# Performance work log

Measured on AMD Instinct MI355X. Metric: run time of the kernel, lower is better.

## Reference

```python
import jax, jax.numpy as jnp
import numpy as np

B, N = 1, 512
NODE_DIM, EDGE_DIM = 384, 128
H, SK, SV, PK, PV = 8, 16, 16, 4, 4
EPS = 1e-8
LN_EPS = 1e-5


def setup_inputs() -> dict:
    key = jax.random.key(0)
    ks = jax.random.split(key, 20)
    d, e = NODE_DIM, EDGE_DIM
    s = 0.02
    rn = lambda k, sh: jax.random.normal(k, sh, jnp.float32) * s
    # orthonormal per-residue rotations (valid rigid frames)
    R, _ = jnp.linalg.qr(jax.random.normal(ks[2], (B, N, 3, 3), jnp.float32))
    out_dim = H * (SV + EDGE_DIM + PV * 4)  # scalar + pairwise + points(3) + point norms(1)
    return dict(
        node_features=jax.random.normal(ks[0], (B, N, d), jnp.float32),
        edge_features=jax.random.normal(ks[1], (B, N, N, e), jnp.float32),
        rotations=R,
        translations=jax.random.normal(ks[3], (B, N, 3), jnp.float32),
        mask=jnp.ones((B, N), bool),
        Wq_s=rn(ks[4], (d, H * SK)), Wk_s=rn(ks[5], (d, H * SK)), Wv_s=rn(ks[6], (d, H * SV)),
        Wq_p=rn(ks[7], (d, H * PK * 3)), Wk_p=rn(ks[8], (d, H * PK * 3)), Wv_p=rn(ks[9], (d, H * PV * 3)),
        point_weights=jnp.full((H,), np.log(np.e - 1.0), jnp.float32),  # softplus -> 1
        Wb=rn(ks[10], (e, H)), bb=jnp.zeros((H,), jnp.float32),
        Wo=rn(ks[11], (out_dim, d)), bo=jnp.zeros((d,), jnp.float32),
        g1=jnp.ones((d,), jnp.float32), beta1=jnp.zeros((d,), jnp.float32),
        W1=rn(ks[12], (d, 2 * d)), b1=jnp.zeros((2 * d,), jnp.float32),
        W2=rn(ks[13], (2 * d, 2 * d)), b2=jnp.zeros((2 * d,), jnp.float32),
        W3=rn(ks[14], (2 * d, d)), b3=jnp.zeros((d,), jnp.float32),
        g2=jnp.ones((d,), jnp.float32), beta2=jnp.zeros((d,), jnp.float32),
    )


def _layer_norm(x, g, b):
    mu = x.mean(-1, keepdims=True)
    var = ((x - mu) ** 2).mean(-1, keepdims=True)
    return (x - mu) * jax.lax.rsqrt(var + LN_EPS) * g + b


def _forward(node_features, edge_features, rotations, translations, mask,
             Wq_s, Wk_s, Wv_s, Wq_p, Wk_p, Wv_p, point_weights, Wb, bb, Wo, bo,
             g1, beta1, W1, b1, W2, b2, W3, b3, g2, beta2):
    b, n, d = node_features.shape
    # num_attn_logits = 3 (scalar + point + pairwise)
    scal_scale = (3 * SK) ** -0.5
    point_scale = (3 * PK * 4.5) ** -0.5
    pair_scale = 3 ** -0.5

    qs = (node_features @ Wq_s).reshape(b, n, H, SK)
    kk = (node_features @ Wk_s).reshape(b, n, H, SK)
    vs = (node_features @ Wv_s).reshape(b, n, H, SV)

    def apply_rigid(p):  # p: (b,n,h,d,3); global = R^T applied per lucidrains einsum + t
        return jnp.einsum('bnhdc,bncr->bnhdr', p, rotations) + translations[:, :, None, None, :]

    qp = apply_rigid((node_features @ Wq_p).reshape(b, n, H, PK, 3))
    kp = apply_rigid((node_features @ Wk_p).reshape(b, n, H, PK, 3))
    vp = apply_rigid((node_features @ Wv_p).reshape(b, n, H, PV, 3))

    logits = jnp.einsum('bihk,bjhk->bhij', qs, kk) * scal_scale

    # point distance term: sum_{d,c} (q-k)^2 = |q|^2 + |k|^2 - 2 q.k (avoids (b,h,i,j,d,3) tensor)
    w = jax.nn.softplus(point_weights)  # (H,)
    q2 = jnp.einsum('bnhdc,bnhdc->bhn', qp, qp)
    k2 = jnp.einsum('bnhdc,bnhdc->bhn', kp, kp)
    cross = jnp.einsum('bihdc,bjhdc->bhij', qp, kp)
    dist = q2[..., :, None] + k2[..., None, :] - 2.0 * cross  # (b,h,i,j)
    logits = logits - 0.5 * point_scale * w[None, :, None, None] * dist

    pair_bias = (jnp.einsum('bije,eh->bhij', edge_features, Wb) + bb[None, :, None, None]) * pair_scale
    logits = logits + pair_bias

    pm = mask[:, None, :, None] & mask[:, None, None, :]  # (b,1,i,j)
    logits = jnp.where(pm, logits, -jnp.finfo(logits.dtype).max)
    attn = jax.nn.softmax(logits, axis=-1)  # (b,h,i,j)

    rs = jnp.einsum('bhij,bjhv->bihv', attn, vs).reshape(b, n, H * SV)
    rp = jnp.einsum('bhij,bije->bihe', attn, edge_features).reshape(b, n, H * EDGE_DIM)
    pts = jnp.einsum('bhij,bjhdc->bihdc', attn, vp)
    # invert rigid: subtract t, apply R (inverse of R^T application)
    local = jnp.einsum('bihdc,birc->bihdr', pts - translations[:, :, None, None, :], rotations)
    norms = jnp.sqrt((local ** 2).sum(-1) + EPS)  # (b,n,H,PV)

    cat = jnp.concatenate([rs, local.reshape(b, n, H * PV * 3), norms.reshape(b, n, H * PV), rp], axis=-1)
    ipa_out = cat @ Wo + bo

    x = _layer_norm(ipa_out, g1, beta1)  # dropout is identity at eval
    x = jax.nn.relu(x @ W1 + b1)
    x = jax.nn.relu(x @ W2 + b2)
    x = x @ W3 + b3
    return _layer_norm(x, g2, beta2)


def reference(node_features, edge_features, rotations, translations, mask,
              Wq_s, Wk_s, Wv_s, Wq_p, Wk_p, Wv_p, point_weights, Wb, bb, Wo, bo,
              g1, beta1, W1, b1, W2, b2, W3, b3, g2, beta2):
    return _forward(node_features, edge_features, rotations, translations, mask,
                    Wq_s, Wk_s, Wv_s, Wq_p, Wk_p, Wv_p, point_weights, Wb, bb, Wo, bo,
                    g1, beta1, W1, b1, W2, b2, W3, b3, g2, beta2)
```

## Files before the change

### kernel.cpp

```cpp
#include <hip/hip_runtime.h>
#include <cstddef>

#define NN 512
#define DD 384
#define EE 128
#define HH 8

static constexpr float SCAL_SCALE  = 0.1443375673f;
static constexpr float POINT_SCALE = 0.1360827635f;
static constexpr float PAIR_SCALE  = 0.5773502692f;
static constexpr float LN_EPS = 1e-5f;
static constexpr float EPS    = 1e-8f;

typedef __bf16 bf16x8 __attribute__((ext_vector_type(8)));
typedef float  f32x4  __attribute__((ext_vector_type(4)));

__device__ __forceinline__ unsigned short bf16_bits(float v) {
    union { __bf16 b; unsigned short s; } c; c.b = (__bf16)v; return c.s;
}
__device__ __forceinline__ float bits2f(unsigned u) {
    union { unsigned u; float f; } c; c.u = u; return c.f;
}

__global__ __launch_bounds__(256) void prep_weights_kernel(
    const float* __restrict__ Wo, const float* __restrict__ W1,
    const float* __restrict__ W2, const float* __restrict__ W3,
    const float* __restrict__ Wq_s, const float* __restrict__ Wk_s,
    const float* __restrict__ Wv_s,
    const float* __restrict__ Wq_p, const float* __restrict__ Wk_p,
    const float* __restrict__ Wv_p,
    unsigned short* __restrict__ WoT, unsigned short* __restrict__ W1T,
    unsigned short* __restrict__ W2T, unsigned short* __restrict__ W3T,
    unsigned short* __restrict__ WprojT)
{
    const int b = blockIdx.x;
    const float* W; unsigned short* out;
    int K, N, tile, rowoff = 0;
    if (b < 480)       { W = Wo;   out = WoT;    K = 1280; N = 384; tile = b; }
    else if (b < 768)  { W = W1;   out = W1T;    K = 384;  N = 768; tile = b - 480; }
    else if (b < 1344) { W = W2;   out = W2T;    K = 768;  N = 768; tile = b - 768; }
    else if (b < 1632) { W = W3;   out = W3T;    K = 768;  N = 384; tile = b - 1344; }
    else if (b < 1680) { W = Wq_s; out = WprojT; K = 384;  N = 128; tile = b - 1632; rowoff = 0; }
    else if (b < 1728) { W = Wk_s; out = WprojT; K = 384;  N = 128; tile = b - 1680; rowoff = 128; }
    else if (b < 1776) { W = Wv_s; out = WprojT; K = 384;  N = 128; tile = b - 1728; rowoff = 256; }
    else if (b < 1812) { W = Wq_p; out = WprojT; K = 384;  N = 96;  tile = b - 1776; rowoff = 384; }
    else if (b < 1848) { W = Wk_p; out = WprojT; K = 384;  N = 96;  tile = b - 1812; rowoff = 480; }
    else               { W = Wv_p; out = WprojT; K = 384;  N = 96;  tile = b - 1848; rowoff = 576; }

    const int ntn = N / 32;
    const int n0 = (tile % ntn) * 32, k0 = (tile / ntn) * 32;
    __shared__ float tb[32][33];
    const int tx = threadIdx.x & 31, ty = threadIdx.x >> 5;
    #pragma unroll
    for (int dy = 0; dy < 32; dy += 8)
        tb[ty + dy][tx] = W[(size_t)(k0 + ty + dy) * N + n0 + tx];
    __syncthreads();
    #pragma unroll
    for (int dy = 0; dy < 32; dy += 8)
        out[(size_t)(rowoff + n0 + ty + dy) * K + k0 + tx] = bf16_bits(tb[tx][ty + dy]);
}

template <int K, int NOUT, bool RELU, bool HASB>
__global__ __launch_bounds__(256) void gemm_mfma2(
    const float* __restrict__ X, const unsigned short* __restrict__ Wt,
    const float* __restrict__ bias, float* __restrict__ Y)
{
    const int t = threadIdx.x;
    const int w = t >> 6, lane = t & 63;
    const int r = lane & 15, q = lane >> 4;
    const int n0 = blockIdx.x * 16;
    const int m0 = blockIdx.y * 64;

    __shared__ unsigned short Xs[64 * 40];
    __shared__ unsigned short Ws[16 * 40];

    const int row_s = t >> 2, seg_s = t & 3;
    f32x4 acc = {0.f, 0.f, 0.f, 0.f};

    for (int ks = 0; ks < K / 32; ks++) {
        __syncthreads();
        {
            const float* src = X + (size_t)(m0 + row_s) * K + ks * 32 + seg_s * 8;
            float4 a = *(const float4*)src;
            float4 b = *(const float4*)(src + 4);
            union { bf16x8 v; uint4 u; } pk;
            pk.v[0] = (__bf16)a.x; pk.v[1] = (__bf16)a.y;
            pk.v[2] = (__bf16)a.z; pk.v[3] = (__bf16)a.w;
            pk.v[4] = (__bf16)b.x; pk.v[5] = (__bf16)b.y;
            pk.v[6] = (__bf16)b.z; pk.v[7] = (__bf16)b.w;
            *(uint4*)&Xs[row_s * 40 + seg_s * 8] = pk.u;
            if (t < 64)
                *(uint4*)&Ws[row_s * 40 + seg_s * 8] =
                    *(const uint4*)&Wt[(size_t)(n0 + row_s) * K + ks * 32 + seg_s * 8];
        }
        __syncthreads();
        bf16x8 a = *(const bf16x8*)&Xs[(w * 16 + r) * 40 + q * 8];
        bf16x8 b = *(const bf16x8*)&Ws[r * 40 + q * 8];
        acc = __builtin_amdgcn_mfma_f32_16x16x32_bf16(a, b, acc, 0, 0, 0);
    }
    const float bi = HASB ? bias[n0 + r] : 0.f;
    #pragma unroll
    for (int reg = 0; reg < 4; reg++) {
        const int m = m0 + w * 16 + q * 4 + reg;
        float v = acc[reg] + bi;
        if (RELU) v = fmaxf(v, 0.f);
        Y[(size_t)m * NOUT + n0 + r] = v;
    }
}

__global__ __launch_bounds__(256) void ipa_post_kernel(
    const float* __restrict__ proj_out, const float* __restrict__ rot,
    const float* __restrict__ trans, const float* __restrict__ pw,
    const float* __restrict__ bb,
    unsigned short* __restrict__ Qp, unsigned short* __restrict__ Kp,
    unsigned short* __restrict__ svT)
{
    const int i = blockIdx.x;
    const int t = threadIdx.x;
    __shared__ float outs[672];
    __shared__ float ptg[288];
    __shared__ float q2s[8], k2s[8], pwh[8];

    for (int f = t; f < 672; f += 256) outs[f] = proj_out[(size_t)i * 672 + f];
    if (t < 8) pwh[t] = 0.5f * POINT_SCALE * log1pf(expf(pw[t]));
    __syncthreads();

    for (int f = t; f < 288; f += 256) {
        int which = f / 96, idx = f % 96;
        int hd = idx / 3, r = idx % 3;
        float acc = trans[(size_t)i * 3 + r];
        #pragma unroll
        for (int c = 0; c < 3; c++)
            acc += outs[384 + which * 96 + hd * 3 + c] * rot[(size_t)i * 9 + c * 3 + r];
        ptg[f] = acc;
    }
    __syncthreads();
    if (t < 16) {
        int which = t / 8, h = t % 8;
        float acc = 0.f;
        #pragma unroll
        for (int m = 0; m < 12; m++) {
            float v = ptg[which * 96 + h * 12 + m];
            acc += v * v;
        }
        (which ? k2s : q2s)[h] = acc;
    }
    __syncthreads();

    {
        const int h = t >> 5, d = t & 31;
        float qv, kv;
        if (d < 16)      { qv = outs[h * 16 + d] * SCAL_SCALE; kv = outs[128 + h * 16 + d]; }
        else if (d < 28) { qv = ptg[h * 12 + d - 16] * (2.f * pwh[h]); kv = ptg[96 + h * 12 + d - 16]; }
        else if (d == 28){ qv = -pwh[h] * q2s[h]; kv = 1.f; }
        else if (d == 29){ qv = 1.f; kv = -pwh[h] * k2s[h]; }
        else if (d == 30){ qv = 1.f; kv = bb[h] * PAIR_SCALE; }
        else             { qv = 0.f; kv = 0.f; }
        Qp[((size_t)i * 8 + h) * 32 + d] = bf16_bits(qv);
        Kp[((size_t)i * 8 + h) * 32 + d] = bf16_bits(kv);
    }
    if (t < 128) {
        int h = t >> 4, v = t & 15;
        svT[((size_t)h * 32 + v) * NN + i] = bf16_bits(outs[256 + h * 16 + v]);
    } else if (t < 224) {
        int idx = t - 128, h = idx / 12, m = idx % 12;
        svT[((size_t)h * 32 + 16 + m) * NN + i] = bf16_bits(ptg[192 + idx]);
    }
}

__global__ __launch_bounds__(256) void ipa_fused(
    const float* __restrict__ edge,
    const unsigned short* __restrict__ Qp, const unsigned short* __restrict__ Kp,
    const unsigned short* __restrict__ svT, const float* __restrict__ Wb,
    float* __restrict__ Opart, float* __restrict__ Mpart, float* __restrict__ Lpart)
{
    const int js = blockIdx.x;
    const int it = blockIdx.y;
    const int i0 = it * 8;
    const int jbase = js * 64;
    const int t = threadIdx.x;
    const int w = t >> 6, lane = t & 63;
    const int r = lane & 15, q = lane >> 4;

    __shared__ unsigned short edA[8 * 8 * 128];
    __shared__ unsigned short wbT[16 * 128];
    __shared__ unsigned short svj[8 * 28 * 8];
    __shared__ float Lb[8 * 8 * 9];
    __shared__ float mrow[64], lrow[64], arow[64];

    for (int idx = t; idx < 2048; idx += 256) {
        int h = idx >> 7, e = idx & 127;
        float v = (h < 8) ? Wb[e * 8 + h] * PAIR_SCALE : 0.f;
        wbT[h * 128 + e] = bf16_bits(v);
    }
    if (t < 64) { mrow[t] = -1e30f; lrow[t] = 0.f; }
    __syncthreads();

    bf16x8 wbf[4];
    #pragma unroll
    for (int s = 0; s < 4; s++)
        wbf[s] = *(const bf16x8*)&wbT[r * 128 + s * 32 + q * 8];

    bf16x8 aq[2];
    #pragma unroll
    for (int hh = 0; hh < 2; hh++)
        aq[hh] = *(const bf16x8*)&Qp[((size_t)(i0 + (r & 7)) * 8 + (w * 2 + hh)) * 32 + q * 8];

    const int ai = t >> 5, hgrp = (t >> 4) & 1, ec = t & 15;
    float rp_acc[4][8];
    #pragma unroll
    for (int a = 0; a < 4; a++)
        #pragma unroll
        for (int e = 0; e < 8; e++) rp_acc[a][e] = 0.f;
    const int l32 = t & 31;
    float sv_acc[7];
    int sh[7], sc[7];
    #pragma unroll
    for (int s = 0; s < 7; s++) {
        int g = l32 * 7 + s;
        sh[s] = g / 28; sc[s] = g % 28;
        sv_acc[s] = 0.f;
    }

    const int sj = t >> 5, sih = (t >> 4) & 1, sseg = t & 15;

    for (int st = 0; st < 8; st++) {
        const int j0 = jbase + st * 8;
        __syncthreads();

        #pragma unroll
        for (int il = 0; il < 4; il++) {
            const int si = sih * 4 + il;
            const float* src = edge + (((size_t)(i0 + si) * NN) + (j0 + sj)) * EE + sseg * 8;
            float4 x0 = *(const float4*)src;
            float4 x1 = *(const float4*)(src + 4);
            union { bf16x8 v; uint4 u; } pk;
            pk.v[0] = (__bf16)x0.x; pk.v[1] = (__bf16)x0.y;
            pk.v[2] = (__bf16)x0.z; pk.v[3] = (__bf16)x0.w;
            pk.v[4] = (__bf16)x1.x; pk.v[5] = (__bf16)x1.y;
            pk.v[6] = (__bf16)x1.z; pk.v[7] = (__bf16)x1.w;
            const int row = sj * 8 + si;
            const int cp = sseg ^ (row & 15);
            *(uint4*)&edA[row * 128 + cp * 8] = pk.u;
        }
        if (t < 224) {
            const int h = t / 28, c = t % 28;
            *(uint4*)&svj[(h * 28 + c) * 8] =
                *(const uint4*)&svT[(size_t)(h * 32 + c) * NN + j0];
        }
        __syncthreads();

        {
            f32x4 acc = {0.f, 0.f, 0.f, 0.f};
            #pragma unroll
            for (int s = 0; s < 4; s++) {
                bf16x8 a = *(const bf16x8*)&edA[(w * 16 + r) * 128 + (((s * 4 + q) ^ r) * 8)];
                acc = __builtin_amdgcn_mfma_f32_16x16x32_bf16(a, wbf[s], acc, 0, 0, 0);
            }
            if (r < 8) {
                #pragma unroll
                for (int reg = 0; reg < 4; reg++) {
                    const int m = q * 4 + reg;
                    Lb[(r * 8 + (m & 7)) * 9 + (w * 2 + (m >> 3))] = acc[reg];
                }
            }
        }
        __syncthreads();

        #pragma unroll
        for (int hh = 0; hh < 2; hh++) {
            const int h = w * 2 + hh;
            bf16x8 bk = *(const bf16x8*)&Kp[((size_t)(j0 + (r & 7)) * 8 + h) * 32 + q * 8];
            f32x4 acc = {0.f, 0.f, 0.f, 0.f};
            acc = __builtin_amdgcn_mfma_f32_16x16x32_bf16(aq[hh], bk, acc, 0, 0, 0);
            if (r < 8 && q < 2) {
                #pragma unroll
                for (int reg = 0; reg < 4; reg++)
                    Lb[(h * 8 + q * 4 + reg) * 9 + r] += acc[reg];
            }
        }
        __syncthreads();

        if (t < 64) {
            float lg[8];
            #pragma unroll
            for (int j = 0; j < 8; j++) lg[j] = Lb[t * 9 + j];
            float mx = lg[0];
            #pragma unroll
            for (int j = 1; j < 8; j++) mx = fmaxf(mx, lg[j]);
            const float mold = mrow[t];
            const float mnew = fmaxf(mold, mx);
            const float al = expf(mold - mnew);
            float sum = 0.f;
            #pragma unroll
            for (int j = 0; j < 8; j++) {
                float p = expf(lg[j] - mnew);
                Lb[t * 9 + j] = p;
                sum += p;
            }
            lrow[t] = lrow[t] * al + sum;
            mrow[t] = mnew;
            arow[t] = al;
        }
        __syncthreads();

        #pragma unroll
        for (int a = 0; a < 4; a++) {
            const float al = arow[(hgrp * 4 + a) * 8 + ai];
            #pragma unroll
            for (int e = 0; e < 8; e++) rp_acc[a][e] *= al;
        }
        #pragma unroll
        for (int s = 0; s < 7; s++) sv_acc[s] *= arow[sh[s] * 8 + ai];

        #pragma unroll
        for (int j = 0; j < 8; j++) {
            const int row = j * 8 + ai;
            uint4 ev = *(const uint4*)&edA[row * 128 + ((ec ^ (row & 15)) * 8)];
            float ef[8];
            ef[0] = bits2f(ev.x << 16); ef[1] = bits2f(ev.x & 0xffff0000u);
            ef[2] = bits2f(ev.y << 16); ef[3] = bits2f(ev.y & 0xffff0000u);
            ef[4] = bits2f(ev.z << 16); ef[5] = bits2f(ev.z & 0xffff0000u);
            ef[6] = bits2f(ev.w << 16); ef[7] = bits2f(ev.w & 0xffff0000u);
            #pragma unroll
            for (int a = 0; a < 4; a++) {
                const float p = Lb[((hgrp * 4 + a) * 8 + ai) * 9 + j];
                #pragma unroll
                for (int e = 0; e < 8; e++) rp_acc[a][e] += p * ef[e];
            }
            #pragma unroll
            for (int s = 0; s < 7; s++) {
                const float p = Lb[(sh[s] * 8 + ai) * 9 + j];
                const float v = bits2f((unsigned)svj[(sh[s] * 28 + sc[s]) * 8 + j] << 16);
                sv_acc[s] += p * v;
            }
        }
    }

    float* orow = Opart + ((size_t)((js * 64 + it) * 8 + ai)) * 1248;
    #pragma unroll
    for (int a = 0; a < 4; a++) {
        const int h = hgrp * 4 + a;
        #pragma unroll
        for (int e = 0; e < 8; e++)
            orow[h * 156 + 28 + ec * 8 + e] = rp_acc[a][e];
    }
    #pragma unroll
    for (int s = 0; s < 7; s++)
        orow[sh[s] * 156 + sc[s]] = sv_acc[s];
    if (t < 64) {
        Mpart[(size_t)(js * 64 + it) * 64 + t] = mrow[t];
        Lpart[(size_t)(js * 64 + it) * 64 + t] = lrow[t];
    }
}

__global__ __launch_bounds__(256) void ipa_merge(
    const float* __restrict__ Opart, const float* __restrict__ Mpart,
    const float* __restrict__ Lpart, float* __restrict__ cat,
    float* __restrict__ pts)
{
    const int i = blockIdx.x;
    const int itile = i >> 3, il = i & 7;
    const int t = threadIdx.x;
    __shared__ float wn[64];

    if (t < 8) {
        const int h = t;
        float ms[8], ls[8], M = -1e30f;
        #pragma unroll
        for (int s = 0; s < 8; s++) {
            ms[s] = Mpart[(size_t)(s * 64 + itile) * 64 + h * 8 + il];
            ls[s] = Lpart[(size_t)(s * 64 + itile) * 64 + h * 8 + il];
            M = fmaxf(M, ms[s]);
        }
        float denom = 0.f, e[8];
        #pragma unroll
        for (int s = 0; s < 8; s++) { e[s] = expf(ms[s] - M); denom += e[s] * ls[s]; }
        const float inv = 1.f / denom;
        #pragma unroll
        for (int s = 0; s < 8; s++) wn[h * 8 + s] = e[s] * inv;
    }
    __syncthreads();

    for (int col = t; col < 1248; col += 256) {
        const int h = col / 156, c = col % 156;
        float acc = 0.f;
        #pragma unroll
        for (int s = 0; s < 8; s++)
            acc += wn[h * 8 + s] *
                   Opart[((size_t)(s * 64 + itile) * 8 + il) * 1248 + col];
        if (c < 16)      cat[(size_t)i * 1280 + h * 16 + c] = acc;
        else if (c < 28) pts[(size_t)i * 96 + h * 12 + (c - 16)] = acc;
        else             cat[(size_t)i * 1280 + 256 + h * 128 + (c - 28)] = acc;
    }
}

__global__ __launch_bounds__(256) void ipa_local_kernel(
    const float* __restrict__ pts, const float* __restrict__ rot,
    const float* __restrict__ trans, float* __restrict__ cat)
{
    const int t = threadIdx.x;
    const int i = blockIdx.x * 2 + (t >> 7);
    const int l = t & 127;
    const float* tr = trans + (size_t)i * 3;
    const float* R  = rot + (size_t)i * 9;
    const float* P  = pts + (size_t)i * 96;
    if (l < 96) {
        int hd = l / 3, rr = l % 3;
        float acc = 0.f;
        #pragma unroll
        for (int c = 0; c < 3; c++)
            acc += (P[hd * 3 + c] - tr[c]) * R[rr * 3 + c];
        cat[(size_t)i * 1280 + 128 + l] = acc;
    } else {
        int pv = l - 96;
        float s = EPS;
        #pragma unroll
        for (int rr = 0; rr < 3; rr++) {
            float v = 0.f;
            #pragma unroll
            for (int c = 0; c < 3; c++)
                v += (P[pv * 3 + c] - tr[c]) * R[rr * 3 + c];
            s += v * v;
        }
        cat[(size_t)i * 1280 + 224 + pv] = sqrtf(s);
    }
}

__global__ __launch_bounds__(256) void ln_kernel(
    const float* __restrict__ X, const float* __restrict__ g,
    const float* __restrict__ beta, float* __restrict__ Y, int Dim)
{
    __shared__ float red[4];
    __shared__ float bc;
    const int i = blockIdx.x;
    const int t = threadIdx.x;
    const float* x = X + (size_t)i * Dim;

    float s = 0.f;
    for (int k = t; k < Dim; k += 256) s += x[k];
    #pragma unroll
    for (int off = 32; off; off >>= 1) s += __shfl_down(s, off, 64);
    if ((t & 63) == 0) red[t >> 6] = s;
    __syncthreads();
    if (t == 0) bc = red[0] + red[1] + red[2] + red[3];
    __syncthreads();
    const float mu = bc / Dim;

    float v = 0.f;
    for (int k = t; k < Dim; k += 256) { float d = x[k] - mu; v += d * d; }
    #pragma unroll
    for (int off = 32; off; off >>= 1) v += __shfl_down(v, off, 64);
    __syncthreads();
    if ((t & 63) == 0) red[t >> 6] = v;
    __syncthreads();
    if (t == 0) bc = red[0] + red[1] + red[2] + red[3];
    __syncthreads();
    const float rstd = rsqrtf(bc / Dim + LN_EPS);

    for (int k = t; k < Dim; k += 256)
        Y[(size_t)i * Dim + k] = (x[k] - mu) * rstd * g[k] + beta[k];
}

extern "C" void kernel_launch(void* const* d_in, const int* in_sizes, int n_in,
                              void* d_out, int out_size, void* d_ws, size_t ws_size,
                              hipStream_t stream)
{
    const float* nf    = (const float*)d_in[0];
    const float* edge  = (const float*)d_in[1];
    const float* rot   = (const float*)d_in[2];
    const float* trans = (const float*)d_in[3];
    const float* Wq_s = (const float*)d_in[5];
    const float* Wk_s = (const float*)d_in[6];
    const float* Wv_s = (const float*)d_in[7];
    const float* Wq_p = (const float*)d_in[8];
    const float* Wk_p = (const float*)d_in[9];
    const float* Wv_p = (const float*)d_in[10];
    const float* pw   = (const float*)d_in[11];
    const float* Wb   = (const float*)d_in[12];
    const float* bb   = (const float*)d_in[13];
    const float* Wo   = (const float*)d_in[14];
    const float* bo   = (const float*)d_in[15];
    const float* g1   = (const float*)d_in[16];
    const float* be1  = (const float*)d_in[17];
    const float* W1   = (const float*)d_in[18];
    const float* b1   = (const float*)d_in[19];
    const float* W2   = (const float*)d_in[20];
    const float* b2   = (const float*)d_in[21];
    const float* W3   = (const float*)d_in[22];
    const float* b3   = (const float*)d_in[23];
    const float* g2   = (const float*)d_in[24];
    const float* be2  = (const float*)d_in[25];

    float* ws = (float*)d_ws;
    float* cat      = ws;
    float* pts      = cat + 655360;
    float* ipa      = pts + 49152;
    float* x1       = ipa + 196608;
    float* h1       = x1  + 196608;
    float* h2       = h1  + 393216;
    float* y        = h2  + 393216;
    float* proj_out = y   + 196608;
    float* Opart    = proj_out + 344064;
    float* Mpart    = Opart + 5111808;
    float* Lpart    = Mpart + 32768;
    unsigned short* Qp  = (unsigned short*)(Lpart + 32768);
    unsigned short* Kp  = Qp  + 131072;
    unsigned short* svT = Kp  + 131072;
    unsigned short* WoT = svT + 131072;
    unsigned short* W1T = WoT + 491520;
    unsigned short* W2T = W1T + 294912;
    unsigned short* W3T = W2T + 589824;
    unsigned short* WprojT = W3T + 294912;

    prep_weights_kernel<<<1884, 256, 0, stream>>>(Wo, W1, W2, W3,
                                                  Wq_s, Wk_s, Wv_s, Wq_p, Wk_p, Wv_p,
                                                  WoT, W1T, W2T, W3T, WprojT);

    gemm_mfma2<384, 672, false, false><<<dim3(42, 8), 256, 0, stream>>>(nf, WprojT, nullptr, proj_out);

    ipa_post_kernel<<<NN, 256, 0, stream>>>(proj_out, rot, trans, pw, bb, Qp, Kp, svT);

    ipa_fused<<<dim3(8, 64), 256, 0, stream>>>(edge, Qp, Kp, svT, Wb,
                                               Opart, Mpart, Lpart);

    ipa_merge<<<NN, 256, 0, stream>>>(Opart, Mpart, Lpart, cat, pts);
    ipa_local_kernel<<<256, 256, 0, stream>>>(pts, rot, trans, cat);

    gemm_mfma2<1280, 384, false, true><<<dim3(24, 8), 256, 0, stream>>>(cat, WoT, bo, ipa);
    ln_kernel<<<NN, 256, 0, stream>>>(ipa, g1, be1, x1, 384);

    gemm_mfma2<384, 768, true, true><<<dim3(48, 8), 256, 0, stream>>>(x1, W1T, b1, h1);
    gemm_mfma2<768, 768, true, true><<<dim3(48, 8), 256, 0, stream>>>(h1, W2T, b2, h2);
    gemm_mfma2<768, 384, false, true><<<dim3(24, 8), 256, 0, stream>>>(h2, W3T, b3, y);

    ln_kernel<<<NN, 256, 0, stream>>>(y, g2, be2, (float*)d_out, 384);
}
```

Baseline: 375.5 us.

## Split attention over more j-chunks, prefetch edges, store bf16 activations between GEMMs

The fused IPA attention kernel now splits j into 16 chunks of 32 instead of 8 of 64. It precomputes all QK logits for the chunk with MFMA up front and software-prefetches the next edge and value tile into registers while the current one is processed. Each thread now accumulates 32 contiguous edge channels for one (head, row) pair and writes them back vectorized. The GEMMs drop the shared-memory staging and instead read pre-converted bf16 inputs directly from global memory; intermediate activations, node features, LN output and the concat buffer are stored as bf16. The local-frame transform is folded into the merge kernel, and the softmax uses fast exp. Risks: a larger partial-output buffer for the merge to read, more register pressure, and extra bf16 rounding on intermediates.

```diff
diff --git a/kernel.cpp b/kernel.cpp
--- a/kernel.cpp
+++ b/kernel.cpp
@@ -5,6 +5,7 @@
 #define DD 384
 #define EE 128
 #define HH 8
+#define JSPLIT 16
 
 static constexpr float SCAL_SCALE  = 0.1443375673f;
 static constexpr float POINT_SCALE = 0.1360827635f;
@@ -28,12 +29,21 @@
     const float* __restrict__ Wq_s, const float* __restrict__ Wk_s,
     const float* __restrict__ Wv_s,
     const float* __restrict__ Wq_p, const float* __restrict__ Wk_p,
-    const float* __restrict__ Wv_p,
+    const float* __restrict__ Wv_p, const float* __restrict__ nf,
     unsigned short* __restrict__ WoT, unsigned short* __restrict__ W1T,
     unsigned short* __restrict__ W2T, unsigned short* __restrict__ W3T,
-    unsigned short* __restrict__ WprojT)
+    unsigned short* __restrict__ WprojT, unsigned short* __restrict__ nfb)
 {
     const int b = blockIdx.x;
+    if (b >= 1884) {
+        const int idx = (b - 1884) * 1024 + threadIdx.x * 4;
+        float4 v = *(const float4*)(nf + idx);
+        unsigned lo = bf16_bits(v.x) | ((unsigned)bf16_bits(v.y) << 16);
+        unsigned hi = bf16_bits(v.z) | ((unsigned)bf16_bits(v.w) << 16);
+        uint2 pk; pk.x = lo; pk.y = hi;
+        *(uint2*)(nfb + idx) = pk;
+        return;
+    }
     const float* W; unsigned short* out;
     int K, N, tile, rowoff = 0;
     if (b < 480)       { W = Wo;   out = WoT;    K = 1280; N = 384; tile = b; }
@@ -60,51 +70,37 @@
         out[(size_t)(rowoff + n0 + ty + dy) * K + k0 + tx] = bf16_bits(tb[tx][ty + dy]);
 }
 
-template <int K, int NOUT, bool RELU, bool HASB>
-__global__ __launch_bounds__(256) void gemm_mfma2(
-    const float* __restrict__ X, const unsigned short* __restrict__ Wt,
-    const float* __restrict__ bias, float* __restrict__ Y)
+template <int K, int NOUT, bool RELU, bool HASB, bool OUTBF>
+__global__ __launch_bounds__(256) void gemm_bf16(
+    const unsigned short* __restrict__ Xb, const unsigned short* __restrict__ Wt,
+    const float* __restrict__ bias, void* __restrict__ Yv)
 {
     const int t = threadIdx.x;
     const int w = t >> 6, lane = t & 63;
     const int r = lane & 15, q = lane >> 4;
     const int n0 = blockIdx.x * 16;
-    const int m0 = blockIdx.y * 64;
-
-    __shared__ unsigned short Xs[64 * 40];
-    __shared__ unsigned short Ws[16 * 40];
-
-    const int row_s = t >> 2, seg_s = t & 3;
+    const int m0 = blockIdx.y * 64 + w * 16;
+
+    const unsigned short* xrow = Xb + (size_t)(m0 + r) * K + q * 8;
+    const unsigned short* wrow = Wt + (size_t)(n0 + r) * K + q * 8;
+
     f32x4 acc = {0.f, 0.f, 0.f, 0.f};
-
-    for (int ks = 0; ks < K / 32; ks++) {
-        __syncthreads();
-        {
-            const float* src = X + (size_t)(m0 + row_s) * K + ks * 32 + seg_s * 8;
-            float4 a = *(const float4*)src;
-            float4 b = *(const float4*)(src + 4);
-            union { bf16x8 v; uint4 u; } pk;
-            pk.v[0] = (__bf16)a.x; pk.v[1] = (__bf16)a.y;
-            pk.v[2] = (__bf16)a.z; pk.v[3] = (__bf16)a.w;
-            pk.v[4] = (__bf16)b.x; pk.v[5] = (__bf16)b.y;
-            pk.v[6] = (__bf16)b.z; pk.v[7] = (__bf16)b.w;
-            *(uint4*)&Xs[row_s * 40 + seg_s * 8] = pk.u;
-            if (t < 64)
-                *(uint4*)&Ws[row_s * 40 + seg_s * 8] =
-                    *(const uint4*)&Wt[(size_t)(n0 + row_s) * K + ks * 32 + seg_s * 8];
-        }
-        __syncthreads();
-        bf16x8 a = *(const bf16x8*)&Xs[(w * 16 + r) * 40 + q * 8];
-        bf16x8 b = *(const bf16x8*)&Ws[r * 40 + q * 8];
-        acc = __builtin_amdgcn_mfma_f32_16x16x32_bf16(a, b, acc, 0, 0, 0);
-    }
-    const float bi = HASB ? bias[n0 + r] : 0.f;
+    #pragma unroll 4
+    for (int k0 = 0; k0 < K; k0 += 32) {
+        union { uint4 u; bf16x8 v; } au, bu;
+        au.u = *(const uint4*)(xrow + k0);
+        bu.u = *(const uint4*)(wrow + k0);
+        acc = __builtin_amdgcn_mfma_f32_16x16x32_bf16(au.v, bu.v, acc, 0, 0, 0);
+    }
+    const int n = n0 + r;
+    const float bi = HASB ? bias[n] : 0.f;
     #pragma unroll
     for (int reg = 0; reg < 4; reg++) {
-        const int m = m0 + w * 16 + q * 4 + reg;
+        const int m = m0 + q * 4 + reg;
         float v = acc[reg] + bi;
         if (RELU) v = fmaxf(v, 0.f);
-        Y[(size_t)m * NOUT + n0 + r] = v;
+        if (OUTBF) ((unsigned short*)Yv)[(size_t)m * NOUT + n] = bf16_bits(v);
+        else       ((float*)Yv)[(size_t)m * NOUT + n] = v;
     }
 }
 
@@ -168,7 +164,7 @@
     }
 }
 
-__global__ __launch_bounds__(256) void ipa_fused(
+__global__ __launch_bounds__(256, 3) void ipa_fused2(
     const float* __restrict__ edge,
     const unsigned short* __restrict__ Qp, const unsigned short* __restrict__ Kp,
     const unsigned short* __restrict__ svT, const float* __restrict__ Wb,
@@ -177,21 +173,21 @@
     const int js = blockIdx.x;
     const int it = blockIdx.y;
     const int i0 = it * 8;
-    const int jbase = js * 64;
+    const int jbase = js * 32;
     const int t = threadIdx.x;
     const int w = t >> 6, lane = t & 63;
     const int r = lane & 15, q = lane >> 4;
 
-    __shared__ unsigned short edA[8 * 8 * 128];
     __shared__ unsigned short wbT[16 * 128];
-    __shared__ unsigned short svj[8 * 28 * 8];
-    __shared__ float Lb[8 * 8 * 9];
+    __shared__ unsigned short edA[64 * 128];
+    __shared__ float Lqk[64 * 37];
+    __shared__ float Lb[64 * 9];
+    __shared__ unsigned short svj[8 * 8 * 32];
     __shared__ float mrow[64], lrow[64], arow[64];
 
     for (int idx = t; idx < 2048; idx += 256) {
         int h = idx >> 7, e = idx & 127;
-        float v = (h < 8) ? Wb[e * 8 + h] * PAIR_SCALE : 0.f;
-        wbT[h * 128 + e] = bf16_bits(v);
+        wbT[idx] = bf16_bits((h < 8) ? Wb[e * 8 + h] * PAIR_SCALE : 0.f);
     }
     if (t < 64) { mrow[t] = -1e30f; lrow[t] = 0.f; }
     __syncthreads();
@@ -201,52 +197,78 @@
     for (int s = 0; s < 4; s++)
         wbf[s] = *(const bf16x8*)&wbT[r * 128 + s * 32 + q * 8];
 
-    bf16x8 aq[2];
-    #pragma unroll
-    for (int hh = 0; hh < 2; hh++)
-        aq[hh] = *(const bf16x8*)&Qp[((size_t)(i0 + (r & 7)) * 8 + (w * 2 + hh)) * 32 + q * 8];
-
-    const int ai = t >> 5, hgrp = (t >> 4) & 1, ec = t & 15;
-    float rp_acc[4][8];
-    #pragma unroll
-    for (int a = 0; a < 4; a++)
-        #pragma unroll
-        for (int e = 0; e < 8; e++) rp_acc[a][e] = 0.f;
-    const int l32 = t & 31;
-    float sv_acc[7];
-    int sh[7], sc[7];
-    #pragma unroll
-    for (int s = 0; s < 7; s++) {
-        int g = l32 * 7 + s;
-        sh[s] = g / 28; sc[s] = g % 28;
-        sv_acc[s] = 0.f;
+    #pragma unroll
+    for (int hh = 0; hh < 2; hh++) {
+        const int h = w * 2 + hh;
+        bf16x8 aq = *(const bf16x8*)&Qp[((size_t)(i0 + (r & 7)) * 8 + h) * 32 + q * 8];
+        #pragma unroll
+        for (int jt = 0; jt < 2; jt++) {
+            bf16x8 bk = *(const bf16x8*)&Kp[((size_t)(jbase + jt * 16 + r) * 8 + h) * 32 + q * 8];
+            f32x4 acc = {0.f, 0.f, 0.f, 0.f};
+            acc = __builtin_amdgcn_mfma_f32_16x16x32_bf16(aq, bk, acc, 0, 0, 0);
+            if (q < 2) {
+                #pragma unroll
+                for (int reg = 0; reg < 4; reg++)
+                    Lqk[(h * 8 + q * 4 + reg) * 37 + jt * 16 + r] = acc[reg];
+            }
+        }
     }
 
     const int sj = t >> 5, sih = (t >> 4) & 1, sseg = t & 15;
-
-    for (int st = 0; st < 8; st++) {
-        const int j0 = jbase + st * 8;
+    const int hsv = t / 28, csv = t % 28;
+    float4 pf[8];
+    uint4 svpf;
+    {
+        const int j0 = jbase;
+        #pragma unroll
+        for (int il = 0; il < 4; il++) {
+            const float* src = edge + (((size_t)(i0 + sih * 4 + il) * NN) + (j0 + sj)) * EE + sseg * 8;
+            pf[il * 2]     = *(const float4*)src;
+            pf[il * 2 + 1] = *(const float4*)(src + 4);
+        }
+        if (t < 224) svpf = *(const uint4*)&svT[(size_t)(hsv * 32 + csv) * NN + j0];
+    }
+
+    const int ai = t >> 5, ah = (t >> 2) & 7, ap = t & 3;
+    const int prow = ah * 8 + ai;
+    float rp[32];
+    float sva[8];
+    #pragma unroll
+    for (int z = 0; z < 32; z++) rp[z] = 0.f;
+    #pragma unroll
+    for (int s = 0; s < 8; s++) sva[s] = 0.f;
+
+    for (int st = 0; st < 4; st++) {
         __syncthreads();
-
         #pragma unroll
         for (int il = 0; il < 4; il++) {
-            const int si = sih * 4 + il;
-            const float* src = edge + (((size_t)(i0 + si) * NN) + (j0 + sj)) * EE + sseg * 8;
-            float4 x0 = *(const float4*)src;
-            float4 x1 = *(const float4*)(src + 4);
+            const int row = sj * 8 + sih * 4 + il;
             union { bf16x8 v; uint4 u; } pk;
-            pk.v[0] = (__bf16)x0.x; pk.v[1] = (__bf16)x0.y;
-            pk.v[2] = (__bf16)x0.z; pk.v[3] = (__bf16)x0.w;
-            pk.v[4] = (__bf16)x1.x; pk.v[5] = (__bf16)x1.y;
-            pk.v[6] = (__bf16)x1.z; pk.v[7] = (__bf16)x1.w;
-            const int row = sj * 8 + si;
-            const int cp = sseg ^ (row & 15);
-            *(uint4*)&edA[row * 128 + cp * 8] = pk.u;
+            pk.v[0] = (__bf16)pf[il*2].x;   pk.v[1] = (__bf16)pf[il*2].y;
+            pk.v[2] = (__bf16)pf[il*2].z;   pk.v[3] = (__bf16)pf[il*2].w;
+            pk.v[4] = (__bf16)pf[il*2+1].x; pk.v[5] = (__bf16)pf[il*2+1].y;
+            pk.v[6] = (__bf16)pf[il*2+1].z; pk.v[7] = (__bf16)pf[il*2+1].w;
+            *(uint4*)&edA[row * 128 + ((sseg ^ (row & 15)) * 8)] = pk.u;
         }
         if (t < 224) {
-            const int h = t / 28, c = t % 28;
-            *(uint4*)&svj[(h * 28 + c) * 8] =
-                *(const uint4*)&svT[(size_t)(h * 32 + c) * NN + j0];
+            svj[(hsv * 8 + 0) * 32 + csv] = (unsigned short)(svpf.x & 0xffff);
+            svj[(hsv * 8 + 1) * 32 + csv] = (unsigned short)(svpf.x >> 16);
+            svj[(hsv * 8 + 2) * 32 + csv] = (unsigned short)(svpf.y & 0xffff);
+            svj[(hsv * 8 + 3) * 32 + csv] = (unsigned short)(svpf.y >> 16);
+            svj[(hsv * 8 + 4) * 32 + csv] = (unsigned short)(svpf.z & 0xffff);
+            svj[(hsv * 8 + 5) * 32 + csv] = (unsigned short)(svpf.z >> 16);
+            svj[(hsv * 8 + 6) * 32 + csv] = (unsigned short)(svpf.w & 0xffff);
+            svj[(hsv * 8 + 7) * 32 + csv] = (unsigned short)(svpf.w >> 16);
+        }
+        if (st < 3) {
+            const int j0 = jbase + (st + 1) * 8;
+            #pragma unroll
+            for (int il = 0; il < 4; il++) {
+                const float* src = edge + (((size_t)(i0 + sih * 4 + il) * NN) + (j0 + sj)) * EE + sseg * 8;
+                pf[il * 2]     = *(const float4*)src;
+                pf[il * 2 + 1] = *(const float4*)(src + 4);
+            }
+            if (t < 224) svpf = *(const uint4*)&svT[(size_t)(hsv * 32 + csv) * NN + j0];
         }
         __syncthreads();
 
@@ -267,34 +289,20 @@
         }
         __syncthreads();
 
-        #pragma unroll
-        for (int hh = 0; hh < 2; hh++) {
-            const int h = w * 2 + hh;
-            bf16x8 bk = *(const bf16x8*)&Kp[((size_t)(j0 + (r & 7)) * 8 + h) * 32 + q * 8];
-            f32x4 acc = {0.f, 0.f, 0.f, 0.f};
-            acc = __builtin_amdgcn_mfma_f32_16x16x32_bf16(aq[hh], bk, acc, 0, 0, 0);
-            if (r < 8 && q < 2) {
-                #pragma unroll
-                for (int reg = 0; reg < 4; reg++)
-                    Lb[(h * 8 + q * 4 + reg) * 9 + r] += acc[reg];
-            }
-        }
-        __syncthreads();
-
         if (t < 64) {
             float lg[8];
+            float mx = -1e30f;
             #pragma unroll
-            for (int j = 0; j < 8; j++) lg[j] = Lb[t * 9 + j];
-            float mx = lg[0];
-            #pragma unroll
-            for (int j = 1; j < 8; j++) mx = fmaxf(mx, lg[j]);
-            const float mold = mrow[t];
-            const float mnew = fmaxf(mold, mx);
-            const float al = expf(mold - mnew);
+            for (int j = 0; j < 8; j++) {
+                lg[j] = Lb[t * 9 + j] + Lqk[t * 37 + st * 8 + j];
+                mx = fmaxf(mx, lg[j]);
+            }
+            const float mnew = fmaxf(mrow[t], mx);
+            const float al = __expf(mrow[t] - mnew);
             float sum = 0.f;
             #pragma unroll
             for (int j = 0; j < 8; j++) {
-                float p = expf(lg[j] - mnew);
+                float p = __expf(lg[j] - mnew);
                 Lb[t * 9 + j] = p;
                 sum += p;
             }
@@ -304,50 +312,59 @@
         }
         __syncthreads();
 
-        #pragma unroll
-        for (int a = 0; a < 4; a++) {
-            const float al = arow[(hgrp * 4 + a) * 8 + ai];
-            #pragma unroll
-            for (int e = 0; e < 8; e++) rp_acc[a][e] *= al;
-        }
-        #pragma unroll
-        for (int s = 0; s < 7; s++) sv_acc[s] *= arow[sh[s] * 8 + ai];
+        const float al = arow[prow];
+        float pj[8];
+        #pragma unroll
+        for (int j = 0; j < 8; j++) pj[j] = Lb[prow * 9 + j];
+        #pragma unroll
+        for (int z = 0; z < 32; z++) rp[z] *= al;
+        #pragma unroll
+        for (int s = 0; s < 8; s++) sva[s] *= al;
 
         #pragma unroll
         for (int j = 0; j < 8; j++) {
             const int row = j * 8 + ai;
-            uint4 ev = *(const uint4*)&edA[row * 128 + ((ec ^ (row & 15)) * 8)];
-            float ef[8];
-            ef[0] = bits2f(ev.x << 16); ef[1] = bits2f(ev.x & 0xffff0000u);
-            ef[2] = bits2f(ev.y << 16); ef[3] = bits2f(ev.y & 0xffff0000u);
-            ef[4] = bits2f(ev.z << 16); ef[5] = bits2f(ev.z & 0xffff0000u);
-            ef[6] = bits2f(ev.w << 16); ef[7] = bits2f(ev.w & 0xffff0000u);
+            const float p = pj[j];
             #pragma unroll
-            for (int a = 0; a < 4; a++) {
-                const float p = Lb[((hgrp * 4 + a) * 8 + ai) * 9 + j];
-                #pragma unroll
-                for (int e = 0; e < 8; e++) rp_acc[a][e] += p * ef[e];
-            }
-            #pragma unroll
-            for (int s = 0; s < 7; s++) {
-                const float p = Lb[(sh[s] * 8 + ai) * 9 + j];
-                const float v = bits2f((unsigned)svj[(sh[s] * 28 + sc[s]) * 8 + j] << 16);
-                sv_acc[s] += p * v;
-            }
-        }
-    }
-
-    float* orow = Opart + ((size_t)((js * 64 + it) * 8 + ai)) * 1248;
-    #pragma unroll
-    for (int a = 0; a < 4; a++) {
-        const int h = hgrp * 4 + a;
-        #pragma unroll
-        for (int e = 0; e < 8; e++)
-            orow[h * 156 + 28 + ec * 8 + e] = rp_acc[a][e];
-    }
-    #pragma unroll
-    for (int s = 0; s < 7; s++)
-        orow[sh[s] * 156 + sc[s]] = sv_acc[s];
+            for (int u = 0; u < 4; u++) {
+                uint4 ev = *(const uint4*)&edA[row * 128 + (((ap * 4 + u) ^ (row & 15)) * 8)];
+                rp[u*8+0] += p * bits2f(ev.x << 16);
+                rp[u*8+1] += p * bits2f(ev.x & 0xffff0000u);
+                rp[u*8+2] += p * bits2f(ev.y << 16);
+                rp[u*8+3] += p * bits2f(ev.y & 0xffff0000u);
+                rp[u*8+4] += p * bits2f(ev.z << 16);
+                rp[u*8+5] += p * bits2f(ev.z & 0xffff0000u);
+                rp[u*8+6] += p * bits2f(ev.w << 16);
+                rp[u*8+7] += p * bits2f(ev.w & 0xffff0000u);
+            }
+            uint4 sv = *(const uint4*)&svj[(ah * 8 + j) * 32 + ap * 8];
+            sva[0] += p * bits2f(sv.x << 16);
+            sva[1] += p * bits2f(sv.x & 0xffff0000u);
+            sva[2] += p * bits2f(sv.y << 16);
+            sva[3] += p * bits2f(sv.y & 0xffff0000u);
+            sva[4] += p * bits2f(sv.z << 16);
+            sva[5] += p * bits2f(sv.z & 0xffff0000u);
+            sva[6] += p * bits2f(sv.w << 16);
+            sva[7] += p * bits2f(sv.w & 0xffff0000u);
+        }
+    }
+
+    float* orow = Opart + (size_t)((js * 64 + it) * 8 + ai) * 1248;
+    #pragma unroll
+    for (int u = 0; u < 8; u++) {
+        f32x4 vv = {rp[u*4+0], rp[u*4+1], rp[u*4+2], rp[u*4+3]};
+        *(f32x4*)&orow[ah * 156 + 28 + ap * 32 + u * 4] = vv;
+    }
+    {
+        f32x4 v0 = {sva[0], sva[1], sva[2], sva[3]};
+        if (ap < 3) {
+            f32x4 v1 = {sva[4], sva[5], sva[6], sva[7]};
+            *(f32x4*)&orow[ah * 156 + ap * 8]     = v0;
+            *(f32x4*)&orow[ah * 156 + ap * 8 + 4] = v1;
+        } else {
+            *(f32x4*)&orow[ah * 156 + 24] = v0;
+        }
+    }
     if (t < 64) {
         Mpart[(size_t)(js * 64 + it) * 64 + t] = mrow[t];
         Lpart[(size_t)(js * 64 + it) * 64 + t] = lrow[t];
@@ -356,29 +373,30 @@
 
 __global__ __launch_bounds__(256) void ipa_merge(
     const float* __restrict__ Opart, const float* __restrict__ Mpart,
-    const float* __restrict__ Lpart, float* __restrict__ cat,
-    float* __restrict__ pts)
+    const float* __restrict__ Lpart, const float* __restrict__ rot,
+    const float* __restrict__ trans, unsigned short* __restrict__ cat_bf)
 {
     const int i = blockIdx.x;
     const int itile = i >> 3, il = i & 7;
     const int t = threadIdx.x;
-    __shared__ float wn[64];
+    __shared__ float wn[8 * JSPLIT];
+    __shared__ float pts_s[96];
 
     if (t < 8) {
         const int h = t;
-        float ms[8], ls[8], M = -1e30f;
-        #pragma unroll
-        for (int s = 0; s < 8; s++) {
+        float ms[JSPLIT], ls[JSPLIT], M = -1e30f;
+        #pragma unroll
+        for (int s = 0; s < JSPLIT; s++) {
             ms[s] = Mpart[(size_t)(s * 64 + itile) * 64 + h * 8 + il];
             ls[s] = Lpart[(size_t)(s * 64 + itile) * 64 + h * 8 + il];
             M = fmaxf(M, ms[s]);
         }
-        float denom = 0.f, e[8];
-        #pragma unroll
-        for (int s = 0; s < 8; s++) { e[s] = expf(ms[s] - M); denom += e[s] * ls[s]; }
+        float denom = 0.f, e[JSPLIT];
+        #pragma unroll
+        for (int s = 0; s < JSPLIT; s++) { e[s] = __expf(ms[s] - M); denom += e[s] * ls[s]; }
         const float inv = 1.f / denom;
         #pragma unroll
-        for (int s = 0; s < 8; s++) wn[h * 8 + s] = e[s] * inv;
+        for (int s = 0; s < JSPLIT; s++) wn[h * JSPLIT + s] = e[s] * inv;
     }
     __syncthreads();
 
@@ -386,50 +404,43 @@
         const int h = col / 156, c = col % 156;
         float acc = 0.f;
         #pragma unroll
-        for (int s = 0; s < 8; s++)
-            acc += wn[h * 8 + s] *
+        for (int s = 0; s < JSPLIT; s++)
+            acc += wn[h * JSPLIT + s] *
                    Opart[((size_t)(s * 64 + itile) * 8 + il) * 1248 + col];
-        if (c < 16)      cat[(size_t)i * 1280 + h * 16 + c] = acc;
-        else if (c < 28) pts[(size_t)i * 96 + h * 12 + (c - 16)] = acc;
-        else             cat[(size_t)i * 1280 + 256 + h * 128 + (c - 28)] = acc;
-    }
-}
-
-__global__ __launch_bounds__(256) void ipa_local_kernel(
-    const float* __restrict__ pts, const float* __restrict__ rot,
-    const float* __restrict__ trans, float* __restrict__ cat)
-{
-    const int t = threadIdx.x;
-    const int i = blockIdx.x * 2 + (t >> 7);
-    const int l = t & 127;
+        if (c < 16)      cat_bf[(size_t)i * 1280 + h * 16 + c] = bf16_bits(acc);
+        else if (c < 28) pts_s[h * 12 + (c - 16)] = acc;
+        else             cat_bf[(size_t)i * 1280 + 256 + h * 128 + (c - 28)] = bf16_bits(acc);
+    }
+    __syncthreads();
+
     const float* tr = trans + (size_t)i * 3;
     const float* R  = rot + (size_t)i * 9;
-    const float* P  = pts + (size_t)i * 96;
-    if (l < 96) {
-        int hd = l / 3, rr = l % 3;
+    if (t < 96) {
+        int hd = t / 3, rr = t % 3;
         float acc = 0.f;
         #pragma unroll
         for (int c = 0; c < 3; c++)
-            acc += (P[hd * 3 + c] - tr[c]) * R[rr * 3 + c];
-        cat[(size_t)i * 1280 + 128 + l] = acc;
-    } else {
-        int pv = l - 96;
+            acc += (pts_s[hd * 3 + c] - tr[c]) * R[rr * 3 + c];
+        cat_bf[(size_t)i * 1280 + 128 + t] = bf16_bits(acc);
+    } else if (t < 128) {
+        int pv = t - 96;
         float s = EPS;
         #pragma unroll
         for (int rr = 0; rr < 3; rr++) {
             float v = 0.f;
             #pragma unroll
             for (int c = 0; c < 3; c++)
-                v += (P[pv * 3 + c] - tr[c]) * R[rr * 3 + c];
+                v += (pts_s[pv * 3 + c] - tr[c]) * R[rr * 3 + c];
             s += v * v;
         }
-        cat[(size_t)i * 1280 + 224 + pv] = sqrtf(s);
-    }
-}
-
+        cat_bf[(size_t)i * 1280 + 224 + pv] = bf16_bits(sqrtf(s));
+    }
+}
+
+template <bool OUTBF>
 __global__ __launch_bounds__(256) void ln_kernel(
     const float* __restrict__ X, const float* __restrict__ g,
-    const float* __restrict__ beta, float* __restrict__ Y, int Dim)
+    const float* __restrict__ beta, void* __restrict__ Yv, int Dim)
 {
     __shared__ float red[4];
     __shared__ float bc;
@@ -458,8 +469,11 @@
     __syncthreads();
     const float rstd = rsqrtf(bc / Dim + LN_EPS);
 
-    for (int k = t; k < Dim; k += 256)
-        Y[(size_t)i * Dim + k] = (x[k] - mu) * rstd * g[k] + beta[k];
+    for (int k = t; k < Dim; k += 256) {
+        float val = (x[k] - mu) * rstd * g[k] + beta[k];
+        if (OUTBF) ((unsigned short*)Yv)[(size_t)i * Dim + k] = bf16_bits(val);
+        else       ((float*)Yv)[(size_t)i * Dim + k] = val;
+    }
 }
 
 extern "C" void kernel_launch(void* const* d_in, const int* in_sizes, int n_in,
@@ -493,46 +507,45 @@
     const float* be2  = (const float*)d_in[25];
 
     float* ws = (float*)d_ws;
-    float* cat      = ws;
-    float* pts      = cat + 655360;
-    float* ipa      = pts + 49152;
-    float* x1       = ipa + 196608;
-    float* h1       = x1  + 196608;
-    float* h2       = h1  + 393216;
-    float* y        = h2  + 393216;
-    float* proj_out = y   + 196608;
-    float* Opart    = proj_out + 344064;
-    float* Mpart    = Opart + 5111808;
-    float* Lpart    = Mpart + 32768;
-    unsigned short* Qp  = (unsigned short*)(Lpart + 32768);
-    unsigned short* Kp  = Qp  + 131072;
-    unsigned short* svT = Kp  + 131072;
+    float* proj_out = ws;
+    float* ipa   = proj_out + 344064;
+    float* y     = ipa + 196608;
+    float* Opart = y + 196608;
+    float* Mpart = Opart + 10223616;
+    float* Lpart = Mpart + 65536;
+    unsigned short* cat_bf = (unsigned short*)(Lpart + 65536);
+    unsigned short* x1b = cat_bf + 655360;
+    unsigned short* h1b = x1b + 196608;
+    unsigned short* h2b = h1b + 393216;
+    unsigned short* Qp  = h2b + 393216;
+    unsigned short* Kp  = Qp + 131072;
+    unsigned short* svT = Kp + 131072;
     unsigned short* WoT = svT + 131072;
     unsigned short* W1T = WoT + 491520;
     unsigned short* W2T = W1T + 294912;
     unsigned short* W3T = W2T + 589824;
     unsigned short* WprojT = W3T + 294912;
-
-    prep_weights_kernel<<<1884, 256, 0, stream>>>(Wo, W1, W2, W3,
-                                                  Wq_s, Wk_s, Wv_s, Wq_p, Wk_p, Wv_p,
-                                                  WoT, W1T, W2T, W3T, WprojT);
-
-    gemm_mfma2<384, 672, false, false><<<dim3(42, 8), 256, 0, stream>>>(nf, WprojT, nullptr, proj_out);
+    unsigned short* nfb = WprojT + 258048;
+
+    prep_weights_kernel<<<2076, 256, 0, stream>>>(Wo, W1, W2, W3,
+                                                  Wq_s, Wk_s, Wv_s, Wq_p, Wk_p, Wv_p, nf,
+                                                  WoT, W1T, W2T, W3T, WprojT, nfb);
+
+    gemm_bf16<384, 672, false, false, false><<<dim3(42, 8), 256, 0, stream>>>(nfb, WprojT, nullptr, proj_out);
 
     ipa_post_kernel<<<NN, 256, 0, stream>>>(proj_out, rot, trans, pw, bb, Qp, Kp, svT);
 
-    ipa_fused<<<dim3(8, 64), 256, 0, stream>>>(edge, Qp, Kp, svT, Wb,
-                                               Opart, Mpart, Lpart);
-
-    ipa_merge<<<NN, 256, 0, stream>>>(Opart, Mpart, Lpart, cat, pts);
-    ipa_local_kernel<<<256, 256, 0, stream>>>(pts, rot, trans, cat);
-
-    gemm_mfma2<1280, 384, false, true><<<dim3(24, 8), 256, 0, stream>>>(cat, WoT, bo, ipa);
-    ln_kernel<<<NN, 256, 0, stream>>>(ipa, g1, be1, x1, 384);
-
-    gemm_mfma2<384, 768, true, true><<<dim3(48, 8), 256, 0, stream>>>(x1, W1T, b1, h1);
-    gemm_mfma2<768, 768, true, true><<<dim3(48, 8), 256, 0, stream>>>(h1, W2T, b2, h2);
-    gemm_mfma2<768, 384, false, true><<<dim3(24, 8), 256, 0, stream>>>(h2, W3T, b3, y);
-
-    ln_kernel<<<NN, 256, 0, stream>>>(y, g2, be2, (float*)d_out, 384);
-}
+    ipa_fused2<<<dim3(JSPLIT, 64), 256, 0, stream>>>(edge, Qp, Kp, svT, Wb,
+                                                     Opart, Mpart, Lpart);
+
+    ipa_merge<<<NN, 256, 0, stream>>>(Opart, Mpart, Lpart, rot, trans, cat_bf);
+
+    gemm_bf16<1280, 384, false, true, false><<<dim3(24, 8), 256, 0, stream>>>(cat_bf, WoT, bo, ipa);
+    ln_kernel<true><<<NN, 256, 0, stream>>>(ipa, g1, be1, x1b, 384);
+
+    gemm_bf16<384, 768, true, true, true><<<dim3(48, 8), 256, 0, stream>>>(x1b, W1T, b1, h1b);
+    gemm_bf16<768, 768, true, true, true><<<dim3(48, 8), 256, 0, stream>>>(h1b, W2T, b2, h2b);
+    gemm_bf16<768, 384, false, true, false><<<dim3(24, 8), 256, 0, stream>>>(h2b, W3T, b3, y);
+
+    ln_kernel<false><<<NN, 256, 0, stream>>>(y, g2, be2, d_out, 384);
+}
```

Result: slower. 851.9 us (+126.9%).
